# Kernel optimization log

Measured on AMD Instinct MI355X. Metric: run time of the kernel, lower is better.

## Reference

```python
import jax, jax.numpy as jnp
import numpy as np

H = 256        # hidden_size
MAX_LEN = 200  # position table has MAX_LEN+1 rows
B = 4096       # number of sessions


def setup_inputs() -> dict:
    rng = np.random.RandomState(0)
    # ragged session lengths in [10, 100)
    seq_len = rng.randint(10, 100, size=B).astype(np.int64)
    T = int(seq_len.sum())
    # reverse positions: len-1, ..., 1, 0 per session (as the torch code uses)
    reverse_pos = np.concatenate([np.arange(l - 1, -1, -1) for l in seq_len]).astype(np.int64)

    key = jax.random.key(0)
    ks = jax.random.split(key, 8)
    def lin(k, fin, fout):
        # torch Linear init ~ U(-1/sqrt(fin), 1/sqrt(fin)); store as [fin, fout]
        lim = 1.0 / np.sqrt(fin)
        kw, kb = jax.random.split(k)
        W = jax.random.uniform(kw, (fin, fout), jnp.float32, -lim, lim)
        b = jax.random.uniform(kb, (fout,), jnp.float32, -lim, lim)
        return W, b

    hidden = jax.random.normal(ks[0], (T, H), jnp.float32)
    pos_table = jax.random.normal(ks[1], (MAX_LEN + 1, H), jnp.float32)
    W_pos, b_pos = lin(ks[2], 2 * H, H)   # W_pos_inter
    W1, b1 = lin(ks[3], H, H)             # W_1_inter
    W2, b2 = lin(ks[4], H, H)             # W_2_inter
    qw, qb = lin(ks[5], H, 1)             # q_inter

    return {
        "hidden": hidden,
        "pos_table": pos_table,
        "W_pos": W_pos, "b_pos": b_pos,
        "W1": W1, "b1": b1,
        "W2": W2, "b2": b2,
        "qw": qw, "qb": qb,
        "seq_len": jnp.asarray(seq_len),
        "reverse_pos": jnp.asarray(reverse_pos),
    }


def reference(hidden, pos_table, W_pos, b_pos, W1, b1, W2, b2, qw, qb, seq_len, reverse_pos):
    T = hidden.shape[0]
    nb = seq_len.shape[0]
    # segment id per token (sessions are contiguous)
    seg = jnp.repeat(jnp.arange(nb), seq_len, total_repeat_length=T)  # [T]
    # per-session mean, gathered back per token (v_mean_repeat_concat)
    sess_mean = jax.ops.segment_sum(hidden, seg, num_segments=nb)
    sess_mean = sess_mean / seq_len[:, None].astype(hidden.dtype)
    v_mean = sess_mean[seg]                                           # [T, H]
    # position-augmented hidden: tanh(W_pos_inter([hidden; pos_emb]))
    pos_emb = pos_table[reverse_pos]                                  # [T, H]
    pos_hidden = jnp.tanh(jnp.concatenate([hidden, pos_emb], -1) @ W_pos + b_pos)
    # alpha = q_inter(sigmoid(W_1_inter(v_mean) + W_2_inter(pos_hidden)))
    gate = jax.nn.sigmoid(v_mean @ W1 + b1 + pos_hidden @ W2 + b2)
    alpha = gate @ qw + qb                                            # [T, 1]
    # per-session weighted sum of hidden
    h_s = jax.ops.segment_sum(alpha * hidden, seg, num_segments=nb)   # [B, H]
    return h_s
```

## Files before the change

### kernel.cpp

```cpp
#include <hip/hip_runtime.h>
#include <hip/hip_bf16.h>
#include <stdint.h>

#define HD 256
#define BM 64
#define BK 32
#define APAD 8
#define ASTRIDE (HD + APAD)

typedef __bf16 bf16x8 __attribute__((ext_vector_type(8)));
typedef float f32x4 __attribute__((ext_vector_type(4)));
typedef unsigned short ushort8v __attribute__((ext_vector_type(8)));
typedef unsigned short us4 __attribute__((ext_vector_type(4)));

__device__ __forceinline__ unsigned short f2bf(float f) {
    unsigned int x = __float_as_uint(f);
    unsigned int r = (x + 0x7FFFu + ((x >> 16) & 1u)) >> 16;
    return (unsigned short)r;
}

__global__ void scan_kernel(const int* __restrict__ seq_len, int* __restrict__ offsets, int B) {
    __shared__ int sums[256];
    int tid = threadIdx.x;
    int per = (B + 255) / 256;
    int b0 = tid * per;
    int local[32];
    int tot = 0;
    for (int i = 0; i < per && i < 32; ++i) {
        int b = b0 + i;
        int v = (b < B) ? seq_len[b] : 0;
        local[i] = tot;
        tot += v;
    }
    sums[tid] = tot;
    __syncthreads();
    for (int off = 1; off < 256; off <<= 1) {
        int v = (tid >= off) ? sums[tid - off] : 0;
        __syncthreads();
        sums[tid] += v;
        __syncthreads();
    }
    int start = sums[tid] - tot;
    for (int i = 0; i < per && i < 32; ++i) {
        int b = b0 + i;
        if (b < B) offsets[b] = start + local[i];
    }
    if (tid == 255) offsets[B] = sums[255];
}

__global__ void mean_kernel(const float* __restrict__ hidden, const int* __restrict__ offsets,
                            float* __restrict__ mean, int* __restrict__ seg) {
    int b = blockIdx.x;
    int s = offsets[b], e = offsets[b + 1];
    int tid = threadIdx.x;
    for (int t = s + tid; t < e; t += 256) seg[t] = b;
    int g = tid >> 6, c = tid & 63;
    float4 acc = {0.f, 0.f, 0.f, 0.f};
    for (int t = s + g; t < e; t += 4) {
        const float4 v = *reinterpret_cast<const float4*>(hidden + (size_t)t * HD + c * 4);
        acc.x += v.x; acc.y += v.y; acc.z += v.z; acc.w += v.w;
    }
    __shared__ float4 part[4][64];
    part[g][c] = acc;
    __syncthreads();
    if (g == 0) {
        float4 a0 = part[0][c], a1 = part[1][c], a2 = part[2][c], a3 = part[3][c];
        float inv = 1.0f / (float)(e - s);
        float4 m;
        m.x = (a0.x + a1.x + a2.x + a3.x) * inv;
        m.y = (a0.y + a1.y + a2.y + a3.y) * inv;
        m.z = (a0.z + a1.z + a2.z + a3.z) * inv;
        m.w = (a0.w + a1.w + a2.w + a3.w) * inv;
        *reinterpret_cast<float4*>(mean + (size_t)b * HD + c * 4) = m;
    }
}

__global__ void transpose_kernel(const float* __restrict__ Wp, const float* __restrict__ W1,
                                 const float* __restrict__ W2,
                                 unsigned short* __restrict__ WphT, unsigned short* __restrict__ WpbT,
                                 unsigned short* __restrict__ W1T, unsigned short* __restrict__ W2T) {
    int n = blockIdx.x;
    int k = threadIdx.x;
    WphT[n * HD + k] = f2bf(Wp[k * HD + n]);
    WpbT[n * HD + k] = f2bf(Wp[(HD + k) * HD + n]);
    W1T[n * HD + k]  = f2bf(W1[k * HD + n]);
    W2T[n * HD + k]  = f2bf(W2[k * HD + n]);
}

__global__ __launch_bounds__(256) void gemm_bias_kernel(
    const float* __restrict__ A, int M,
    const unsigned short* __restrict__ BT,
    const float* __restrict__ bias1, const float* __restrict__ bias2,
    float* __restrict__ out) {
    __shared__ __align__(16) unsigned short As[BM][ASTRIDE];
    int tid = threadIdx.x;
    int m0 = blockIdx.x * BM;
    int wave = tid >> 6, lane = tid & 63, quad = lane >> 4, cc = lane & 15;
    int nb = wave * 64;
    f32x4 acc[4][4];
    for (int i = 0; i < 4; ++i) for (int j = 0; j < 4; ++j) acc[i][j] = (f32x4){0.f, 0.f, 0.f, 0.f};

    {
        int row = tid >> 2;
        int m = m0 + row;
        for (int i = 0; i < 8; ++i) {
            int cg = ((tid & 3) + 4 * i) * 8;
            float4 f0 = {0,0,0,0}, f1 = {0,0,0,0};
            if (m < M) {
                const float4* p = reinterpret_cast<const float4*>(A + (size_t)m * HD + cg);
                f0 = p[0]; f1 = p[1];
            }
            ushort8v pk;
            pk[0] = f2bf(f0.x); pk[1] = f2bf(f0.y); pk[2] = f2bf(f0.z); pk[3] = f2bf(f0.w);
            pk[4] = f2bf(f1.x); pk[5] = f2bf(f1.y); pk[6] = f2bf(f1.z); pk[7] = f2bf(f1.w);
            *reinterpret_cast<ushort8v*>(&As[row][cg]) = pk;
        }
    }
    __syncthreads();

    for (int kc = 0; kc < HD; kc += BK) {
        bf16x8 bfr[4];
        for (int nf = 0; nf < 4; ++nf)
            bfr[nf] = *reinterpret_cast<const bf16x8*>(BT + (size_t)(nb + nf * 16 + cc) * HD + kc + quad * 8);
        for (int mf = 0; mf < 4; ++mf) {
            bf16x8 af = *reinterpret_cast<const bf16x8*>(&As[mf * 16 + cc][kc + quad * 8]);
            for (int nf = 0; nf < 4; ++nf)
                acc[mf][nf] = __builtin_amdgcn_mfma_f32_16x16x32_bf16(af, bfr[nf], acc[mf][nf], 0, 0, 0);
        }
    }
    for (int mf = 0; mf < 4; ++mf)
        for (int nf = 0; nf < 4; ++nf)
            for (int r = 0; r < 4; ++r) {
                int row = m0 + mf * 16 + quad * 4 + r;
                int col = nb + nf * 16 + cc;
                if (row < M) {
                    float v = acc[mf][nf][r] + bias1[col];
                    if (bias2) v += bias2[col];
                    out[(size_t)row * HD + col] = v;
                }
            }
}

__global__ __launch_bounds__(256, 4) void main_kernel(
    const float* __restrict__ hidden, int T,
    const unsigned short* __restrict__ WphT,
    const unsigned short* __restrict__ W2T,
    const float* __restrict__ P2,
    const float* __restrict__ u,
    const float* __restrict__ qw, const float* __restrict__ qb,
    const int* __restrict__ rp, const int* __restrict__ seg,
    float* __restrict__ alpha) {
    __shared__ __align__(16) unsigned short Ah[BM][ASTRIDE];
    __shared__ int rp_s[BM];
    __shared__ int seg_s[BM];
    __shared__ float alpha_s[BM];

    int tid = threadIdx.x;
    int t0 = blockIdx.x * BM;
    int wave = tid >> 6, lane = tid & 63, quad = lane >> 4, cc = lane & 15;
    int mb = wave * 64;

    {
        int row = tid >> 2;
        int t = t0 + row;
        for (int i = 0; i < 8; ++i) {
            int cg = ((tid & 3) + 4 * i) * 8;
            float4 f0 = {0,0,0,0}, f1 = {0,0,0,0};
            if (t < T) {
                const float4* p = reinterpret_cast<const float4*>(hidden + (size_t)t * HD + cg);
                f0 = p[0]; f1 = p[1];
            }
            ushort8v pk;
            pk[0] = f2bf(f0.x); pk[1] = f2bf(f0.y); pk[2] = f2bf(f0.z); pk[3] = f2bf(f0.w);
            pk[4] = f2bf(f1.x); pk[5] = f2bf(f1.y); pk[6] = f2bf(f1.z); pk[7] = f2bf(f1.w);
            *reinterpret_cast<ushort8v*>(&Ah[row][cg]) = pk;
        }
    }
    if (tid < BM) {
        int t = t0 + tid;
        rp_s[tid]  = (t < T) ? rp[t] : 0;
        seg_s[tid] = (t < T) ? seg[t] : 0;
        alpha_s[tid] = qb[0];
    }
    __syncthreads();

    f32x4 acc[4][4];
    for (int i = 0; i < 4; ++i) for (int j = 0; j < 4; ++j) acc[i][j] = (f32x4){0.f, 0.f, 0.f, 0.f};

    for (int kc = 0; kc < HD; kc += BK) {
        bf16x8 bfr[4];
        for (int nf = 0; nf < 4; ++nf)
            bfr[nf] = *reinterpret_cast<const bf16x8*>(&Ah[nf * 16 + cc][kc + quad * 8]);
        for (int mf = 0; mf < 4; ++mf) {
            bf16x8 af = *reinterpret_cast<const bf16x8*>(WphT + (size_t)(mb + mf * 16 + cc) * HD + kc + quad * 8);
            for (int nf = 0; nf < 4; ++nf)
                acc[mf][nf] = __builtin_amdgcn_mfma_f32_16x16x32_bf16(af, bfr[nf], acc[mf][nf], 0, 0, 0);
        }
    }
    __syncthreads();

    for (int mf = 0; mf < 4; ++mf)
        for (int nf = 0; nf < 4; ++nf) {
            int token = nf * 16 + cc;
            int h0 = mb + mf * 16 + quad * 4;
            const float4 p2v = *reinterpret_cast<const float4*>(P2 + (size_t)rp_s[token] * HD + h0);
            us4 pk;
            {
                float v0 = acc[mf][nf][0] + p2v.x;
                float v1 = acc[mf][nf][1] + p2v.y;
                float v2 = acc[mf][nf][2] + p2v.z;
                float v3 = acc[mf][nf][3] + p2v.w;
                float e0 = __expf(2.f * v0), e1 = __expf(2.f * v1);
                float e2 = __expf(2.f * v2), e3 = __expf(2.f * v3);
                pk[0] = f2bf(1.f - 2.f / (e0 + 1.f));
                pk[1] = f2bf(1.f - 2.f / (e1 + 1.f));
                pk[2] = f2bf(1.f - 2.f / (e2 + 1.f));
                pk[3] = f2bf(1.f - 2.f / (e3 + 1.f));
            }
            *reinterpret_cast<us4*>(&Ah[token][h0]) = pk;
            acc[mf][nf] = (f32x4){0.f, 0.f, 0.f, 0.f};
        }
    __syncthreads();

    for (int kc = 0; kc < HD; kc += BK) {
        bf16x8 bfr[4];
        for (int nf = 0; nf < 4; ++nf)
            bfr[nf] = *reinterpret_cast<const bf16x8*>(W2T + (size_t)(mb + nf * 16 + cc) * HD + kc + quad * 8);
        for (int mf = 0; mf < 4; ++mf) {
            bf16x8 af = *reinterpret_cast<const bf16x8*>(&Ah[mf * 16 + cc][kc + quad * 8]);
            for (int nf = 0; nf < 4; ++nf)
                acc[mf][nf] = __builtin_amdgcn_mfma_f32_16x16x32_bf16(af, bfr[nf], acc[mf][nf], 0, 0, 0);
        }
    }

    float qwv[4];
    for (int nf = 0; nf < 4; ++nf) qwv[nf] = qw[mb + nf * 16 + cc];
    for (int mf = 0; mf < 4; ++mf)
        for (int r = 0; r < 4; ++r) {
            int token = mf * 16 + quad * 4 + r;
            const float* urow = u + (size_t)seg_s[token] * HD;
            float s = 0.f;
            for (int nf = 0; nf < 4; ++nf) {
                float g = acc[mf][nf][r] + urow[mb + nf * 16 + cc];
                g = 1.0f / (1.0f + __expf(-g));
                s += g * qwv[nf];
            }
            s += __shfl_xor(s, 1);
            s += __shfl_xor(s, 2);
            s += __shfl_xor(s, 4);
            s += __shfl_xor(s, 8);
            if (cc == 0) atomicAdd(&alpha_s[token], s);
        }
    __syncthreads();
    if (tid < BM) {
        int t = t0 + tid;
        if (t < T) alpha[t] = alpha_s[tid];
    }
}

__global__ void hs_kernel(const float* __restrict__ hidden, const float* __restrict__ alpha,
                          const int* __restrict__ offsets, float* __restrict__ out) {
    int b = blockIdx.x;
    int s = offsets[b], e = offsets[b + 1];
    int tid = threadIdx.x;
    __shared__ float al[256];
    for (int i = tid; i < e - s; i += 256) al[i] = alpha[s + i];
    __syncthreads();
    int g = tid >> 6, c = tid & 63;
    float4 acc = {0.f, 0.f, 0.f, 0.f};
    for (int t = s + g; t < e; t += 4) {
        float a = al[t - s];
        const float4 v = *reinterpret_cast<const float4*>(hidden + (size_t)t * HD + c * 4);
        acc.x += a * v.x; acc.y += a * v.y; acc.z += a * v.z; acc.w += a * v.w;
    }
    __shared__ float4 part[4][64];
    part[g][c] = acc;
    __syncthreads();
    if (g == 0) {
        float4 a0 = part[0][c], a1 = part[1][c], a2 = part[2][c], a3 = part[3][c];
        float4 m;
        m.x = a0.x + a1.x + a2.x + a3.x;
        m.y = a0.y + a1.y + a2.y + a3.y;
        m.z = a0.z + a1.z + a2.z + a3.z;
        m.w = a0.w + a1.w + a2.w + a3.w;
        *reinterpret_cast<float4*>(out + (size_t)b * HD + c * 4) = m;
    }
}

extern "C" void kernel_launch(void* const* d_in, const int* in_sizes, int n_in,
                              void* d_out, int out_size, void* d_ws, size_t ws_size,
                              hipStream_t stream) {
    (void)n_in; (void)out_size; (void)ws_size;
    const float* hidden    = (const float*)d_in[0];
    const float* pos_table = (const float*)d_in[1];
    const float* W_pos     = (const float*)d_in[2];
    const float* b_pos     = (const float*)d_in[3];
    const float* W1        = (const float*)d_in[4];
    const float* b1        = (const float*)d_in[5];
    const float* W2        = (const float*)d_in[6];
    const float* b2        = (const float*)d_in[7];
    const float* qw        = (const float*)d_in[8];
    const float* qb        = (const float*)d_in[9];
    const int* seq_len     = (const int*)d_in[10];
    const int* reverse_pos = (const int*)d_in[11];

    int T  = in_sizes[0] / HD;
    int B  = in_sizes[10];
    int NP = in_sizes[1] / HD;

    char* ws = (char*)d_ws;
    auto carve = [&](size_t bytes) -> char* {
        char* p = ws;
        ws += (bytes + 255) & ~(size_t)255;
        return p;
    };
    int* offsets         = (int*)carve((size_t)(B + 1) * sizeof(int));
    int* seg             = (int*)carve((size_t)T * sizeof(int));
    float* mean          = (float*)carve((size_t)B * HD * sizeof(float));
    float* u             = (float*)carve((size_t)B * HD * sizeof(float));
    float* P2            = (float*)carve((size_t)NP * HD * sizeof(float));
    unsigned short* WphT = (unsigned short*)carve((size_t)HD * HD * 2);
    unsigned short* WpbT = (unsigned short*)carve((size_t)HD * HD * 2);
    unsigned short* W1T  = (unsigned short*)carve((size_t)HD * HD * 2);
    unsigned short* W2T  = (unsigned short*)carve((size_t)HD * HD * 2);
    float* alpha         = (float*)carve((size_t)T * sizeof(float));

    scan_kernel<<<1, 256, 0, stream>>>(seq_len, offsets, B);
    transpose_kernel<<<HD, HD, 0, stream>>>(W_pos, W1, W2, WphT, WpbT, W1T, W2T);
    mean_kernel<<<B, 256, 0, stream>>>(hidden, offsets, mean, seg);
    gemm_bias_kernel<<<(NP + BM - 1) / BM, 256, 0, stream>>>(pos_table, NP, WpbT, b_pos, nullptr, P2);
    gemm_bias_kernel<<<(B + BM - 1) / BM, 256, 0, stream>>>(mean, B, W1T, b1, b2, u);
    main_kernel<<<(T + BM - 1) / BM, 256, 0, stream>>>(hidden, T, WphT, W2T, P2, u, qw, qb,
                                                       reverse_pos, seg, alpha);
    hs_kernel<<<B, 256, 0, stream>>>(hidden, alpha, offsets, (float*)d_out);
}
```

Baseline: 594.2 us.

## Cache bf16 copy of hidden in workspace, merge small GEMMs, prefetch weight fragments

The mean kernel now also writes a bf16 copy of hidden into the workspace, when it fits, and stores the session means as bf16. The main kernel and the final weighted-sum kernel read that half-size copy instead of re-reading and converting fp32 hidden. This trades one extra write pass for two half-size read passes. The two small GEMMs (pos_table projection and mean projection) are merged into one launch with 16-row tiles. Weight fragments are register-prefetched one K-step ahead, and main_kernel occupancy hint drops from 4 to 3 blocks. The final h_s sum now uses bf16-rounded hidden, which lowers output precision.

```diff
diff --git a/kernel.cpp b/kernel.cpp
--- a/kernel.cpp
+++ b/kernel.cpp
@@ -4,7 +4,6 @@
 
 #define HD 256
 #define BM 64
-#define BK 32
 #define APAD 8
 #define ASTRIDE (HD + APAD)
 
@@ -49,7 +48,8 @@
 }
 
 __global__ void mean_kernel(const float* __restrict__ hidden, const int* __restrict__ offsets,
-                            float* __restrict__ mean, int* __restrict__ seg) {
+                            unsigned short* __restrict__ mean_bf, unsigned short* __restrict__ hb,
+                            int* __restrict__ seg) {
     int b = blockIdx.x;
     int s = offsets[b], e = offsets[b + 1];
     int tid = threadIdx.x;
@@ -59,6 +59,11 @@
     for (int t = s + g; t < e; t += 4) {
         const float4 v = *reinterpret_cast<const float4*>(hidden + (size_t)t * HD + c * 4);
         acc.x += v.x; acc.y += v.y; acc.z += v.z; acc.w += v.w;
+        if (hb) {
+            us4 pk;
+            pk[0] = f2bf(v.x); pk[1] = f2bf(v.y); pk[2] = f2bf(v.z); pk[3] = f2bf(v.w);
+            *reinterpret_cast<us4*>(hb + (size_t)t * HD + c * 4) = pk;
+        }
     }
     __shared__ float4 part[4][64];
     part[g][c] = acc;
@@ -66,12 +71,12 @@
     if (g == 0) {
         float4 a0 = part[0][c], a1 = part[1][c], a2 = part[2][c], a3 = part[3][c];
         float inv = 1.0f / (float)(e - s);
-        float4 m;
-        m.x = (a0.x + a1.x + a2.x + a3.x) * inv;
-        m.y = (a0.y + a1.y + a2.y + a3.y) * inv;
-        m.z = (a0.z + a1.z + a2.z + a3.z) * inv;
-        m.w = (a0.w + a1.w + a2.w + a3.w) * inv;
-        *reinterpret_cast<float4*>(mean + (size_t)b * HD + c * 4) = m;
+        us4 pk;
+        pk[0] = f2bf((a0.x + a1.x + a2.x + a3.x) * inv);
+        pk[1] = f2bf((a0.y + a1.y + a2.y + a3.y) * inv);
+        pk[2] = f2bf((a0.z + a1.z + a2.z + a3.z) * inv);
+        pk[3] = f2bf((a0.w + a1.w + a2.w + a3.w) * inv);
+        *reinterpret_cast<us4*>(mean_bf + (size_t)b * HD + c * 4) = pk;
     }
 }
 
@@ -87,62 +92,81 @@
     W2T[n * HD + k]  = f2bf(W2[k * HD + n]);
 }
 
-__global__ __launch_bounds__(256) void gemm_bias_kernel(
-    const float* __restrict__ A, int M,
-    const unsigned short* __restrict__ BT,
-    const float* __restrict__ bias1, const float* __restrict__ bias2,
-    float* __restrict__ out) {
-    __shared__ __align__(16) unsigned short As[BM][ASTRIDE];
+__global__ __launch_bounds__(256) void small_gemm_kernel(
+    const unsigned short* __restrict__ mean_bf, int Mu, int nbu,
+    const float* __restrict__ pos_table, int Mp,
+    const unsigned short* __restrict__ W1T, const unsigned short* __restrict__ WpbT,
+    const float* __restrict__ b1, const float* __restrict__ b2, const float* __restrict__ bp,
+    float* __restrict__ u, float* __restrict__ P2) {
+    __shared__ __align__(16) unsigned short As[16][ASTRIDE];
     int tid = threadIdx.x;
-    int m0 = blockIdx.x * BM;
+    bool isU = (int)blockIdx.x < nbu;
+    int m0 = isU ? blockIdx.x * 16 : (blockIdx.x - nbu) * 16;
+    int M  = isU ? Mu : Mp;
+    const unsigned short* BT = isU ? W1T : WpbT;
+    float* out = isU ? u : P2;
+
+    {
+        int row = tid >> 4;
+        int colg = (tid & 15) * 16;
+        int m = m0 + row;
+        if (isU) {
+            ushort8v v0 = {0,0,0,0,0,0,0,0}, v1 = {0,0,0,0,0,0,0,0};
+            if (m < M) {
+                v0 = *reinterpret_cast<const ushort8v*>(mean_bf + (size_t)m * HD + colg);
+                v1 = *reinterpret_cast<const ushort8v*>(mean_bf + (size_t)m * HD + colg + 8);
+            }
+            *reinterpret_cast<ushort8v*>(&As[row][colg])     = v0;
+            *reinterpret_cast<ushort8v*>(&As[row][colg + 8]) = v1;
+        } else {
+            float4 f[4] = {{0,0,0,0},{0,0,0,0},{0,0,0,0},{0,0,0,0}};
+            if (m < M) {
+                const float4* p = reinterpret_cast<const float4*>(pos_table + (size_t)m * HD + colg);
+                f[0] = p[0]; f[1] = p[1]; f[2] = p[2]; f[3] = p[3];
+            }
+            ushort8v v0, v1;
+            v0[0]=f2bf(f[0].x); v0[1]=f2bf(f[0].y); v0[2]=f2bf(f[0].z); v0[3]=f2bf(f[0].w);
+            v0[4]=f2bf(f[1].x); v0[5]=f2bf(f[1].y); v0[6]=f2bf(f[1].z); v0[7]=f2bf(f[1].w);
+            v1[0]=f2bf(f[2].x); v1[1]=f2bf(f[2].y); v1[2]=f2bf(f[2].z); v1[3]=f2bf(f[2].w);
+            v1[4]=f2bf(f[3].x); v1[5]=f2bf(f[3].y); v1[6]=f2bf(f[3].z); v1[7]=f2bf(f[3].w);
+            *reinterpret_cast<ushort8v*>(&As[row][colg])     = v0;
+            *reinterpret_cast<ushort8v*>(&As[row][colg + 8]) = v1;
+        }
+    }
+    __syncthreads();
+
     int wave = tid >> 6, lane = tid & 63, quad = lane >> 4, cc = lane & 15;
     int nb = wave * 64;
-    f32x4 acc[4][4];
-    for (int i = 0; i < 4; ++i) for (int j = 0; j < 4; ++j) acc[i][j] = (f32x4){0.f, 0.f, 0.f, 0.f};
-
-    {
-        int row = tid >> 2;
-        int m = m0 + row;
-        for (int i = 0; i < 8; ++i) {
-            int cg = ((tid & 3) + 4 * i) * 8;
-            float4 f0 = {0,0,0,0}, f1 = {0,0,0,0};
-            if (m < M) {
-                const float4* p = reinterpret_cast<const float4*>(A + (size_t)m * HD + cg);
-                f0 = p[0]; f1 = p[1];
-            }
-            ushort8v pk;
-            pk[0] = f2bf(f0.x); pk[1] = f2bf(f0.y); pk[2] = f2bf(f0.z); pk[3] = f2bf(f0.w);
-            pk[4] = f2bf(f1.x); pk[5] = f2bf(f1.y); pk[6] = f2bf(f1.z); pk[7] = f2bf(f1.w);
-            *reinterpret_cast<ushort8v*>(&As[row][cg]) = pk;
-        }
-    }
-    __syncthreads();
-
-    for (int kc = 0; kc < HD; kc += BK) {
-        bf16x8 bfr[4];
+    f32x4 acc4[4];
+    for (int i = 0; i < 4; ++i) acc4[i] = (f32x4){0.f, 0.f, 0.f, 0.f};
+
+    bf16x8 wfp[4];
+    for (int nf = 0; nf < 4; ++nf)
+        wfp[nf] = *reinterpret_cast<const bf16x8*>(BT + (size_t)(nb + nf * 16 + cc) * HD + quad * 8);
+    for (int kc8 = 0; kc8 < 8; ++kc8) {
+        int kc = kc8 * 32;
+        bf16x8 wfc[4];
+        for (int nf = 0; nf < 4; ++nf) wfc[nf] = wfp[nf];
+        if (kc8 < 7)
+            for (int nf = 0; nf < 4; ++nf)
+                wfp[nf] = *reinterpret_cast<const bf16x8*>(BT + (size_t)(nb + nf * 16 + cc) * HD + kc + 32 + quad * 8);
+        bf16x8 af = *reinterpret_cast<const bf16x8*>(&As[cc][kc + quad * 8]);
         for (int nf = 0; nf < 4; ++nf)
-            bfr[nf] = *reinterpret_cast<const bf16x8*>(BT + (size_t)(nb + nf * 16 + cc) * HD + kc + quad * 8);
-        for (int mf = 0; mf < 4; ++mf) {
-            bf16x8 af = *reinterpret_cast<const bf16x8*>(&As[mf * 16 + cc][kc + quad * 8]);
-            for (int nf = 0; nf < 4; ++nf)
-                acc[mf][nf] = __builtin_amdgcn_mfma_f32_16x16x32_bf16(af, bfr[nf], acc[mf][nf], 0, 0, 0);
-        }
-    }
-    for (int mf = 0; mf < 4; ++mf)
-        for (int nf = 0; nf < 4; ++nf)
-            for (int r = 0; r < 4; ++r) {
-                int row = m0 + mf * 16 + quad * 4 + r;
-                int col = nb + nf * 16 + cc;
-                if (row < M) {
-                    float v = acc[mf][nf][r] + bias1[col];
-                    if (bias2) v += bias2[col];
-                    out[(size_t)row * HD + col] = v;
-                }
-            }
-}
-
-__global__ __launch_bounds__(256, 4) void main_kernel(
-    const float* __restrict__ hidden, int T,
+            acc4[nf] = __builtin_amdgcn_mfma_f32_16x16x32_bf16(af, wfc[nf], acc4[nf], 0, 0, 0);
+    }
+    for (int nf = 0; nf < 4; ++nf)
+        for (int r = 0; r < 4; ++r) {
+            int row = m0 + quad * 4 + r;
+            int col = nb + nf * 16 + cc;
+            if (row < M) {
+                float bias = isU ? (b1[col] + b2[col]) : bp[col];
+                out[(size_t)row * HD + col] = acc4[nf][r] + bias;
+            }
+        }
+}
+
+__global__ __launch_bounds__(256, 3) void main_kernel(
+    const float* __restrict__ hidden, const unsigned short* __restrict__ hb, int T,
     const unsigned short* __restrict__ WphT,
     const unsigned short* __restrict__ W2T,
     const float* __restrict__ P2,
@@ -160,20 +184,33 @@
     int wave = tid >> 6, lane = tid & 63, quad = lane >> 4, cc = lane & 15;
     int mb = wave * 64;
 
+    bf16x8 afp[4];
+    for (int mf = 0; mf < 4; ++mf)
+        afp[mf] = *reinterpret_cast<const bf16x8*>(WphT + (size_t)(mb + mf * 16 + cc) * HD + quad * 8);
+
     {
         int row = tid >> 2;
         int t = t0 + row;
-        for (int i = 0; i < 8; ++i) {
-            int cg = ((tid & 3) + 4 * i) * 8;
-            float4 f0 = {0,0,0,0}, f1 = {0,0,0,0};
-            if (t < T) {
-                const float4* p = reinterpret_cast<const float4*>(hidden + (size_t)t * HD + cg);
-                f0 = p[0]; f1 = p[1];
-            }
-            ushort8v pk;
-            pk[0] = f2bf(f0.x); pk[1] = f2bf(f0.y); pk[2] = f2bf(f0.z); pk[3] = f2bf(f0.w);
-            pk[4] = f2bf(f1.x); pk[5] = f2bf(f1.y); pk[6] = f2bf(f1.z); pk[7] = f2bf(f1.w);
-            *reinterpret_cast<ushort8v*>(&Ah[row][cg]) = pk;
+        if (hb) {
+            for (int i = 0; i < 8; ++i) {
+                int cg = (tid & 3) * 8 + 32 * i;
+                ushort8v v = {0,0,0,0,0,0,0,0};
+                if (t < T) v = *reinterpret_cast<const ushort8v*>(hb + (size_t)t * HD + cg);
+                *reinterpret_cast<ushort8v*>(&Ah[row][cg]) = v;
+            }
+        } else {
+            for (int i = 0; i < 8; ++i) {
+                int cg = (tid & 3) * 8 + 32 * i;
+                float4 f0 = {0,0,0,0}, f1 = {0,0,0,0};
+                if (t < T) {
+                    const float4* p = reinterpret_cast<const float4*>(hidden + (size_t)t * HD + cg);
+                    f0 = p[0]; f1 = p[1];
+                }
+                ushort8v pk;
+                pk[0] = f2bf(f0.x); pk[1] = f2bf(f0.y); pk[2] = f2bf(f0.z); pk[3] = f2bf(f0.w);
+                pk[4] = f2bf(f1.x); pk[5] = f2bf(f1.y); pk[6] = f2bf(f1.z); pk[7] = f2bf(f1.w);
+                *reinterpret_cast<ushort8v*>(&Ah[row][cg]) = pk;
+            }
         }
     }
     if (tid < BM) {
@@ -187,17 +224,25 @@
     f32x4 acc[4][4];
     for (int i = 0; i < 4; ++i) for (int j = 0; j < 4; ++j) acc[i][j] = (f32x4){0.f, 0.f, 0.f, 0.f};
 
-    for (int kc = 0; kc < HD; kc += BK) {
+    for (int kc8 = 0; kc8 < 8; ++kc8) {
+        int kc = kc8 * 32;
+        bf16x8 afc[4];
+        for (int mf = 0; mf < 4; ++mf) afc[mf] = afp[mf];
+        if (kc8 < 7)
+            for (int mf = 0; mf < 4; ++mf)
+                afp[mf] = *reinterpret_cast<const bf16x8*>(WphT + (size_t)(mb + mf * 16 + cc) * HD + kc + 32 + quad * 8);
         bf16x8 bfr[4];
         for (int nf = 0; nf < 4; ++nf)
             bfr[nf] = *reinterpret_cast<const bf16x8*>(&Ah[nf * 16 + cc][kc + quad * 8]);
-        for (int mf = 0; mf < 4; ++mf) {
-            bf16x8 af = *reinterpret_cast<const bf16x8*>(WphT + (size_t)(mb + mf * 16 + cc) * HD + kc + quad * 8);
+        for (int mf = 0; mf < 4; ++mf)
             for (int nf = 0; nf < 4; ++nf)
-                acc[mf][nf] = __builtin_amdgcn_mfma_f32_16x16x32_bf16(af, bfr[nf], acc[mf][nf], 0, 0, 0);
-        }
-    }
-    __syncthreads();
+                acc[mf][nf] = __builtin_amdgcn_mfma_f32_16x16x32_bf16(afc[mf], bfr[nf], acc[mf][nf], 0, 0, 0);
+    }
+    __syncthreads();
+
+    bf16x8 wfp[4];
+    for (int nf = 0; nf < 4; ++nf)
+        wfp[nf] = *reinterpret_cast<const bf16x8*>(W2T + (size_t)(mb + nf * 16 + cc) * HD + quad * 8);
 
     for (int mf = 0; mf < 4; ++mf)
         for (int nf = 0; nf < 4; ++nf) {
@@ -222,14 +267,17 @@
         }
     __syncthreads();
 
-    for (int kc = 0; kc < HD; kc += BK) {
-        bf16x8 bfr[4];
-        for (int nf = 0; nf < 4; ++nf)
-            bfr[nf] = *reinterpret_cast<const bf16x8*>(W2T + (size_t)(mb + nf * 16 + cc) * HD + kc + quad * 8);
+    for (int kc8 = 0; kc8 < 8; ++kc8) {
+        int kc = kc8 * 32;
+        bf16x8 wfc[4];
+        for (int nf = 0; nf < 4; ++nf) wfc[nf] = wfp[nf];
+        if (kc8 < 7)
+            for (int nf = 0; nf < 4; ++nf)
+                wfp[nf] = *reinterpret_cast<const bf16x8*>(W2T + (size_t)(mb + nf * 16 + cc) * HD + kc + 32 + quad * 8);
         for (int mf = 0; mf < 4; ++mf) {
             bf16x8 af = *reinterpret_cast<const bf16x8*>(&Ah[mf * 16 + cc][kc + quad * 8]);
             for (int nf = 0; nf < 4; ++nf)
-                acc[mf][nf] = __builtin_amdgcn_mfma_f32_16x16x32_bf16(af, bfr[nf], acc[mf][nf], 0, 0, 0);
+                acc[mf][nf] = __builtin_amdgcn_mfma_f32_16x16x32_bf16(af, wfc[nf], acc[mf][nf], 0, 0, 0);
         }
     }
 
@@ -258,7 +306,8 @@
     }
 }
 
-__global__ void hs_kernel(const float* __restrict__ hidden, const float* __restrict__ alpha,
+__global__ void hs_kernel(const float* __restrict__ hidden, const unsigned short* __restrict__ hb,
+                          const float* __restrict__ alpha,
                           const int* __restrict__ offsets, float* __restrict__ out) {
     int b = blockIdx.x;
     int s = offsets[b], e = offsets[b + 1];
@@ -268,10 +317,21 @@
     __syncthreads();
     int g = tid >> 6, c = tid & 63;
     float4 acc = {0.f, 0.f, 0.f, 0.f};
-    for (int t = s + g; t < e; t += 4) {
-        float a = al[t - s];
-        const float4 v = *reinterpret_cast<const float4*>(hidden + (size_t)t * HD + c * 4);
-        acc.x += a * v.x; acc.y += a * v.y; acc.z += a * v.z; acc.w += a * v.w;
+    if (hb) {
+        for (int t = s + g; t < e; t += 4) {
+            float a = al[t - s];
+            us4 v = *reinterpret_cast<const us4*>(hb + (size_t)t * HD + c * 4);
+            acc.x += a * __uint_as_float(((unsigned)v[0]) << 16);
+            acc.y += a * __uint_as_float(((unsigned)v[1]) << 16);
+            acc.z += a * __uint_as_float(((unsigned)v[2]) << 16);
+            acc.w += a * __uint_as_float(((unsigned)v[3]) << 16);
+        }
+    } else {
+        for (int t = s + g; t < e; t += 4) {
+            float a = al[t - s];
+            const float4 v = *reinterpret_cast<const float4*>(hidden + (size_t)t * HD + c * 4);
+            acc.x += a * v.x; acc.y += a * v.y; acc.z += a * v.z; acc.w += a * v.w;
+        }
     }
     __shared__ float4 part[4][64];
     part[g][c] = acc;
@@ -290,7 +350,7 @@
 extern "C" void kernel_launch(void* const* d_in, const int* in_sizes, int n_in,
                               void* d_out, int out_size, void* d_ws, size_t ws_size,
                               hipStream_t stream) {
-    (void)n_in; (void)out_size; (void)ws_size;
+    (void)n_in; (void)out_size;
     const float* hidden    = (const float*)d_in[0];
     const float* pos_table = (const float*)d_in[1];
     const float* W_pos     = (const float*)d_in[2];
@@ -309,28 +369,35 @@
     int NP = in_sizes[1] / HD;
 
     char* ws = (char*)d_ws;
+    char* ws_end = ws + ws_size;
     auto carve = [&](size_t bytes) -> char* {
         char* p = ws;
         ws += (bytes + 255) & ~(size_t)255;
         return p;
     };
-    int* offsets         = (int*)carve((size_t)(B + 1) * sizeof(int));
-    int* seg             = (int*)carve((size_t)T * sizeof(int));
-    float* mean          = (float*)carve((size_t)B * HD * sizeof(float));
-    float* u             = (float*)carve((size_t)B * HD * sizeof(float));
-    float* P2            = (float*)carve((size_t)NP * HD * sizeof(float));
-    unsigned short* WphT = (unsigned short*)carve((size_t)HD * HD * 2);
-    unsigned short* WpbT = (unsigned short*)carve((size_t)HD * HD * 2);
-    unsigned short* W1T  = (unsigned short*)carve((size_t)HD * HD * 2);
-    unsigned short* W2T  = (unsigned short*)carve((size_t)HD * HD * 2);
-    float* alpha         = (float*)carve((size_t)T * sizeof(float));
+    int* offsets          = (int*)carve((size_t)(B + 1) * sizeof(int));
+    int* seg              = (int*)carve((size_t)T * sizeof(int));
+    unsigned short* meanb = (unsigned short*)carve((size_t)B * HD * 2);
+    float* u              = (float*)carve((size_t)B * HD * sizeof(float));
+    float* P2             = (float*)carve((size_t)NP * HD * sizeof(float));
+    unsigned short* WphT  = (unsigned short*)carve((size_t)HD * HD * 2);
+    unsigned short* WpbT  = (unsigned short*)carve((size_t)HD * HD * 2);
+    unsigned short* W1T   = (unsigned short*)carve((size_t)HD * HD * 2);
+    unsigned short* W2T   = (unsigned short*)carve((size_t)HD * HD * 2);
+    float* alpha          = (float*)carve((size_t)T * sizeof(float));
+    unsigned short* hb    = nullptr;
+    if ((size_t)(ws_end - ws) >= (size_t)T * HD * 2 + 256)
+        hb = (unsigned short*)carve((size_t)T * HD * 2);
+
+    int nbu = (B + 15) / 16;
+    int nbp = (NP + 15) / 16;
 
     scan_kernel<<<1, 256, 0, stream>>>(seq_len, offsets, B);
     transpose_kernel<<<HD, HD, 0, stream>>>(W_pos, W1, W2, WphT, WpbT, W1T, W2T);
-    mean_kernel<<<B, 256, 0, stream>>>(hidden, offsets, mean, seg);
-    gemm_bias_kernel<<<(NP + BM - 1) / BM, 256, 0, stream>>>(pos_table, NP, WpbT, b_pos, nullptr, P2);
-    gemm_bias_kernel<<<(B + BM - 1) / BM, 256, 0, stream>>>(mean, B, W1T, b1, b2, u);
-    main_kernel<<<(T + BM - 1) / BM, 256, 0, stream>>>(hidden, T, WphT, W2T, P2, u, qw, qb,
+    mean_kernel<<<B, 256, 0, stream>>>(hidden, offsets, meanb, hb, seg);
+    small_gemm_kernel<<<nbu + nbp, 256, 0, stream>>>(meanb, B, nbu, pos_table, NP,
+                                                     W1T, WpbT, b1, b2, b_pos, u, P2);
+    main_kernel<<<(T + BM - 1) / BM, 256, 0, stream>>>(hidden, hb, T, WphT, W2T, P2, u, qw, qb,
                                                        reverse_pos, seg, alpha);
-    hs_kernel<<<B, 256, 0, stream>>>(hidden, alpha, offsets, (float*)d_out);
-}
+    hs_kernel<<<B, 256, 0, stream>>>(hidden, hb, alpha, offsets, (float*)d_out);
+}
```

Measured after the change: 575.5 us. 3.1% less time.
